# Performance work log

Measured on AMD Instinct MI355X. Metric: run time of the kernel, lower is better.

Reference implementation:

```python
import jax, jax.numpy as jnp
import numpy as np

N, E, D, B = 40000, 100000, 64, 256

def setup_inputs() -> dict:
    key = jax.random.key(0)
    ks = jax.random.split(key, 32)
    p = lambda k, shp: jax.random.normal(k, shp, dtype=jnp.float32) * 0.1
    inp = {
        'n_feat': jax.random.normal(ks[0], (N, 23), dtype=jnp.float32),
        'e_feat': jax.random.normal(ks[1], (E, 19), dtype=jnp.float32),
        'src': jax.random.randint(ks[2], (E,), 0, N, dtype=jnp.int32),
        'dst': jax.random.randint(ks[3], (E,), 0, N, dtype=jnp.int32),
        'node_graph': jnp.sort(jax.random.randint(ks[4], (N,), 0, B, dtype=jnp.int32)),
        'batch_size': B,
        'lin0_w': p(ks[5], (D, 23)), 'lin0_b': p(ks[6], (D,)),
        'en_w1': p(ks[7], (128, 19)), 'en_b1': p(ks[8], (128,)),
        'en_w2': p(ks[9], (D * D, 128)), 'en_b2': p(ks[10], (D * D,)),
        'conv_b': p(ks[11], (D,)),
        'gru_wih': p(ks[12], (3 * D, D)), 'gru_whh': p(ks[13], (3 * D, D)),
        'gru_bih': p(ks[14], (3 * D,)), 'gru_bhh': p(ks[15], (3 * D,)),
        'ls_wih0': p(ks[16], (4 * D, 2 * D)), 'ls_wih12': p(ks[17], (2, 4 * D, D)),
        'ls_whh': p(ks[18], (3, 4 * D, D)),
        'ls_bih': p(ks[19], (3, 4 * D)), 'ls_bhh': p(ks[20], (3, 4 * D)),
        'lin3_w': p(ks[21], (2 * D, 2 * D)), 'lin3_b': p(ks[22], (2 * D,)),
        'pred_w': p(ks[23], (1, 2 * D)), 'pred_b': p(ks[24], (1,)),
    }
    return inp


def _gru_step(x, h, wih, whh, bih, bhh):
    gi = x @ wih.T + bih   # (N, 3D)
    gh = h @ whh.T + bhh
    i_r, i_z, i_n = jnp.split(gi, 3, axis=-1)
    h_r, h_z, h_n = jnp.split(gh, 3, axis=-1)
    r = jax.nn.sigmoid(i_r + h_r)
    z = jax.nn.sigmoid(i_z + h_z)
    n = jnp.tanh(i_n + r * h_n)
    return (1.0 - z) * n + z * h


def _lstm_cell(x, h, c, wih, whh, bih, bhh):
    g = x @ wih.T + bih + h @ whh.T + bhh  # (B, 4D)
    i, f, gg, o = jnp.split(g, 4, axis=-1)
    c2 = jax.nn.sigmoid(f) * c + jax.nn.sigmoid(i) * jnp.tanh(gg)
    h2 = jax.nn.sigmoid(o) * jnp.tanh(c2)
    return h2, c2


def reference(n_feat, e_feat, src, dst, node_graph, batch_size,
              lin0_w, lin0_b, en_w1, en_b1, en_w2, en_b2, conv_b,
              gru_wih, gru_whh, gru_bih, gru_bhh,
              ls_wih0, ls_wih12, ls_whh, ls_bih, ls_bhh,
              lin3_w, lin3_b, pred_w, pred_b):
    d = lin0_b.shape[0]
    n_nodes = n_feat.shape[0]
    # input projection
    out = n_feat @ lin0_w.T + lin0_b                       # (N, D)
    h = out                                                # GRU hidden (1 layer)
    # edge network (same every step) -> per-edge weight matrices
    ew = jax.nn.relu(e_feat @ en_w1.T + en_b1) @ en_w2.T + en_b2
    ew = ew.reshape(-1, d, d)                              # (E, D, D)
    for _ in range(6):
        msg = jnp.einsum('ed,edf->ef', out[src], ew)       # gather + per-edge GEMM
        m = jax.ops.segment_sum(msg, dst, num_segments=n_nodes) + conv_b
        h = _gru_step(m, h, gru_wih, gru_whh, gru_bih, gru_bhh)
        out = h
    # Set2Set pooling
    hs = [jnp.zeros((batch_size, d), jnp.float32) for _ in range(3)]
    cs = [jnp.zeros((batch_size, d), jnp.float32) for _ in range(3)]
    q_star = jnp.zeros((batch_size, 2 * d), jnp.float32)
    for _ in range(6):
        x = q_star
        for l in range(3):
            wih = ls_wih0 if l == 0 else ls_wih12[l - 1]
            hs[l], cs[l] = _lstm_cell(x, hs[l], cs[l], wih, ls_whh[l], ls_bih[l], ls_bhh[l])
            x = hs[l]
        q = x                                              # (B, D)
        e = jnp.sum(out * q[node_graph], axis=-1)          # (N,)
        emax = jax.ops.segment_max(e, node_graph, num_segments=batch_size)
        ee = jnp.exp(e - emax[node_graph])
        esum = jax.ops.segment_sum(ee, node_graph, num_segments=batch_size)
        alpha = (ee / esum[node_graph])[:, None]
        readout = jax.ops.segment_sum(out * alpha, node_graph, num_segments=batch_size)
        q_star = jnp.concatenate([q, readout], axis=-1)
    y = jax.nn.relu(q_star @ lin3_w.T + lin3_b)
    predict = y @ pred_w.T + pred_b
    return h[None], predict
```

## Files before the change

kernel.cpp:

```cpp
#include <hip/hip_runtime.h>

typedef unsigned short u16;
typedef unsigned int u32;
typedef _Float16 f16;
typedef __attribute__((ext_vector_type(8))) _Float16 f16x8;
typedef __attribute__((ext_vector_type(4))) _Float16 f16x4;
typedef __attribute__((ext_vector_type(4))) float f32x4;

#define NN 40000
#define EE 100000
#define DD 64
#define BB 256
#define XTS 136
#define EPB 128

__device__ inline float sigmoidf_(float x){
    return 1.f / (1.f + __expf(-x));
}
__device__ inline float tanhf_(float x){
    x = fmaxf(fminf(x, 15.f), -15.f);
    float e = __expf(2.f * x);
    return (e - 1.f) / (e + 1.f);
}

typedef __attribute__((address_space(3))) unsigned int lds_u32;
typedef __attribute__((address_space(1))) const unsigned int g_u32;
__device__ inline void gload_lds16(const void* g, void* l){
    __builtin_amdgcn_global_load_lds((g_u32*)g, (lds_u32*)l, 16, 0, 0);
}

__global__ __launch_bounds__(256) void prep_kernel(
    const float* __restrict__ en_w2, f16* __restrict__ w2h,
    const float* __restrict__ gru_wih, const float* __restrict__ gru_whh,
    f16* __restrict__ wf16h, f16* __restrict__ wf16l,
    const float* __restrict__ ls_wih0, const float* __restrict__ ls_wih12,
    const float* __restrict__ ls_whh, float* __restrict__ lsT,
    const float* __restrict__ lin3_w, float* __restrict__ lin3T,
    const float* __restrict__ gru_bih, const float* __restrict__ conv_b,
    float* __restrict__ effb,
    const int* __restrict__ node_graph, int* __restrict__ offs)
{
    int i = blockIdx.x * 256 + threadIdx.x;
    if (i < 524288){
        w2h[i] = (f16)en_w2[i];
        return;
    }
    i -= 524288;
    if (i < 49152){
        int sel = i / 12288;
        int r = i % 12288;
        int gg = sel >> 1, islo = sel & 1;
        float v = (gg ? gru_whh : gru_wih)[r];
        f16 hi = (f16)v;
        if (islo) wf16l[gg * 12288 + r] = (f16)(v - (float)hi);
        else      wf16h[gg * 12288 + r] = hi;
        return;
    }
    i -= 49152;
    if (i < 114688){
        float v;
        if (i < 32768){
            int d = i >> 8, g = i & 255;
            v = ls_wih0[g * 128 + d];
        } else if (i < 65536){
            int j = i - 32768;
            int l = j >> 14, r = j & 16383;
            int d = r >> 8, g = r & 255;
            v = ls_wih12[l * 16384 + g * 64 + d];
        } else {
            int j = i - 65536;
            int l = j >> 14, r = j & 16383;
            int d = r >> 8, g = r & 255;
            v = ls_whh[l * 16384 + g * 64 + d];
        }
        lsT[i] = v;
        return;
    }
    i -= 114688;
    if (i < 16384){
        int ii = i >> 7, jj = i & 127;
        lin3T[i] = lin3_w[jj * 128 + ii];
        return;
    }
    i -= 16384;
    if (i < 192){
        float b = gru_bih[i];
        #pragma unroll
        for (int d = 0; d < 64; d++) b += gru_wih[i * 64 + d] * conv_b[d];
        effb[i] = b;
        return;
    }
    i -= 192;
    if (i <= 256){
        int lo = 0, hi = NN;
        while (lo < hi){
            int mid = (lo + hi) >> 1;
            if (node_graph[mid] < i) lo = mid + 1; else hi = mid;
        }
        offs[i] = lo;
        return;
    }
}

__global__ __launch_bounds__(256) void lin0_kernel(
    const float* __restrict__ nf, const float* __restrict__ w,
    const float* __restrict__ b, float* __restrict__ out)
{
    int tid = blockIdx.x * 256 + threadIdx.x;
    int n = tid >> 6, d = tid & 63;
    if (n >= NN) return;
    float acc = b[d];
    const float* nr = nf + (size_t)n * 23;
    const float* wr = w + d * 23;
    #pragma unroll
    for (int j = 0; j < 23; j++) acc = fmaf(nr[j], wr[j], acc);
    out[(size_t)n * 64 + d] = acc;
}

__global__ __launch_bounds__(256) void edge_hidden_kernel(
    const float* __restrict__ ef, const float* __restrict__ w1,
    const float* __restrict__ b1, f16* __restrict__ hidh)
{
    int tid = blockIdx.x * 256 + threadIdx.x;
    int e = tid >> 7, k = tid & 127;
    if (e >= EE) return;
    float acc = b1[k];
    const float* er = ef + (size_t)e * 19;
    const float* wr = w1 + k * 19;
    #pragma unroll
    for (int j = 0; j < 19; j++) acc = fmaf(er[j], wr[j], acc);
    acc = fmaxf(acc, 0.f);
    hidh[(size_t)e * 128 + k] = (f16)acc;
}

__global__ __launch_bounds__(512) void msg_fused_kernel(
    const float* __restrict__ h, const f16* __restrict__ hidh,
    const f16* __restrict__ w2h, const float* __restrict__ b2,
    const int* __restrict__ src, const int* __restrict__ dst,
    float* __restrict__ m)
{
    __shared__ f16 s_xT[64 * XTS];
    __shared__ f16 s_b2f[4096];
    __shared__ int s_dst[EPB];
    __shared__ f16x8 s_t0[1024], s_t1[1024], s_t2[1024];

    const int t = threadIdx.x;
    const int base = blockIdx.x * EPB;
    const int lane = t & 63;
    const int wid = t >> 6;

    int goff[2], lbase[2];
    #pragma unroll
    for (int cc = 0; cc < 2; cc++){
        int s = cc * 512 + wid * 64 + lane;
        int kh = s >> 9;
        int c2 = s & 511;
        int col = c2 >> 3;
        int jj = (c2 & 7) ^ (col & 7);
        goff[cc] = col * 128 + kh * 64 + jj * 8;
        lbase[cc] = cc * 512 + wid * 64;
    }

#define STG_ISSUE(DN, BUF)                                                   \
    {                                                                        \
        const f16* gsrc = w2h + (size_t)(DN) * 8192;                         \
        gload_lds16(gsrc + goff[0], (BUF) + lbase[0]);                       \
        gload_lds16(gsrc + goff[1], (BUF) + lbase[1]);                       \
    }

    f16x8* pb0 = s_t0;
    f16x8* pb1 = s_t1;
    f16x8* pb2 = s_t2;
    STG_ISSUE(0, pb0);
    STG_ISSUE(1, pb1);

    for (int i = t; i < EPB * 64; i += 512){
        int el = i >> 6, f = i & 63;
        int e = base + el;
        float v = 0.f;
        if (e < EE) v = h[(size_t)src[e] * 64 + f];
        s_xT[f * XTS + el] = (f16)v;
    }
    for (int i = t; i < 4096; i += 512) s_b2f[i] = (f16)b2[i];
    if (t < EPB){
        int e = base + t;
        s_dst[t] = (e < EE) ? dst[e] : -1;
    }

    const int eg = wid >> 1;
    const int fp = wid & 1;
    const int r16 = lane & 15;
    const int kg = lane >> 4;
    const int we = eg * 32;
    const int sw = r16 & 7;

    f16x8 ah[2][4];
    #pragma unroll
    for (int mt = 0; mt < 2; mt++){
        int e = base + we + mt * 16 + r16;
        #pragma unroll
        for (int ks = 0; ks < 4; ks++){
            if (e < EE){
                ah[mt][ks] = *(const f16x8*)(hidh + (size_t)e * 128 + ks * 32 + kg * 8);
            } else {
                f16x8 z = {0,0,0,0,0,0,0,0};
                ah[mt][ks] = z;
            }
        }
    }

    f32x4 msg[2][2];
    #pragma unroll
    for (int a = 0; a < 2; a++)
        #pragma unroll
        for (int b = 0; b < 2; b++){
            f32x4 z = {0.f, 0.f, 0.f, 0.f};
            msg[a][b] = z;
        }

    int rslot[2][4];
    #pragma unroll
    for (int ftl = 0; ftl < 2; ftl++){
        int col = fp * 32 + ftl * 16 + r16;
        #pragma unroll
        for (int ks = 0; ks < 4; ks++){
            int j2 = (ks & 1) * 4 + kg;
            rslot[ftl][ks] = (ks >> 1) * 512 + col * 8 + (j2 ^ sw);
        }
    }

    __syncthreads();

    for (int d = 0; d < 64; d++){
        if (d + 2 < 64) STG_ISSUE(d + 2, pb2);
        f32x4 xv[2];
        #pragma unroll
        for (int mt = 0; mt < 2; mt++){
            f16x4 xh = *(const f16x4*)&s_xT[d * XTS + we + mt * 16 + kg * 4];
            #pragma unroll
            for (int r = 0; r < 4; r++) xv[mt][r] = (float)xh[r];
        }
        __builtin_amdgcn_s_setprio(1);
        #pragma unroll
        for (int ftl = 0; ftl < 2; ftl++){
            f16x8 bf0 = pb0[rslot[ftl][0]];
            f16x8 bf1 = pb0[rslot[ftl][1]];
            f16x8 bf2 = pb0[rslot[ftl][2]];
            f16x8 bf3 = pb0[rslot[ftl][3]];
            float b2v = (float)s_b2f[d * 64 + fp * 32 + ftl * 16 + r16];
            #pragma unroll
            for (int mt = 0; mt < 2; mt++){
                f32x4 acc = {b2v, b2v, b2v, b2v};
                acc = __builtin_amdgcn_mfma_f32_16x16x32_f16(ah[mt][0], bf0, acc, 0, 0, 0);
                acc = __builtin_amdgcn_mfma_f32_16x16x32_f16(ah[mt][1], bf1, acc, 0, 0, 0);
                acc = __builtin_amdgcn_mfma_f32_16x16x32_f16(ah[mt][2], bf2, acc, 0, 0, 0);
                acc = __builtin_amdgcn_mfma_f32_16x16x32_f16(ah[mt][3], bf3, acc, 0, 0, 0);
                msg[mt][ftl] = xv[mt] * acc + msg[mt][ftl];
            }
        }
        __builtin_amdgcn_s_setprio(0);
        if (d < 63){
            if (d <= 61) asm volatile("s_waitcnt vmcnt(2)" ::: "memory");
            else         asm volatile("s_waitcnt vmcnt(0)" ::: "memory");
            __builtin_amdgcn_s_barrier();
        }
        f16x8* tmp = pb0; pb0 = pb1; pb1 = pb2; pb2 = tmp;
    }
#undef STG_ISSUE

    #pragma unroll
    for (int mt = 0; mt < 2; mt++){
        #pragma unroll
        for (int r = 0; r < 4; r++){
            int el = we + mt * 16 + kg * 4 + r;
            int dt = s_dst[el];
            if (dt >= 0){
                #pragma unroll
                for (int ftl = 0; ftl < 2; ftl++)
                    atomicAdd(&m[(size_t)dt * 64 + fp * 32 + ftl * 16 + r16],
                              msg[mt][ftl][r]);
            }
        }
    }
}

__global__ __launch_bounds__(256) void gru_mfma_kernel(
    float* __restrict__ m, float* __restrict__ h,
    const f16* __restrict__ wf16h, const f16* __restrict__ wf16l,
    const float* __restrict__ effb, const float* __restrict__ bhh)
{
    __shared__ float s_g[2][32][194];
    const int t = threadIdx.x;
    const int base = blockIdx.x * 32;
    const int lane = t & 63;
    const int wid = t >> 6;
    const int rt = wid & 1;
    const int gg = wid >> 1;
    const int r16 = lane & 15;
    const int kg = lane >> 4;

    const float* __restrict__ X = gg ? h : m;
    int n = base + rt * 16 + r16;

    f16x8 ah[2], al[2];
    #pragma unroll
    for (int ks = 0; ks < 2; ks++){
        const float* xp = X + (size_t)n * 64 + ks * 32 + kg * 8;
        f32x4 v0 = *(const f32x4*)(xp);
        f32x4 v1 = *(const f32x4*)(xp + 4);
        #pragma unroll
        for (int j = 0; j < 4; j++){
            f16 hi0 = (f16)v0[j], hi1 = (f16)v1[j];
            ah[ks][j] = hi0;     ah[ks][4 + j] = hi1;
            al[ks][j] = (f16)(v0[j] - (float)hi0);
            al[ks][4 + j] = (f16)(v1[j] - (float)hi1);
        }
    }

    const f16* __restrict__ wh = wf16h + gg * 12288;
    const f16* __restrict__ wl = wf16l + gg * 12288;
    #pragma unroll
    for (int ct = 0; ct < 12; ct++){
        int g = ct * 16 + r16;
        f16x8 bh0 = *(const f16x8*)(wh + g * 64 + kg * 8);
        f16x8 bh1 = *(const f16x8*)(wh + g * 64 + 32 + kg * 8);
        f16x8 bl0 = *(const f16x8*)(wl + g * 64 + kg * 8);
        f16x8 bl1 = *(const f16x8*)(wl + g * 64 + 32 + kg * 8);
        f32x4 acc = {0.f, 0.f, 0.f, 0.f};
        acc = __builtin_amdgcn_mfma_f32_16x16x32_f16(ah[0], bh0, acc, 0, 0, 0);
        acc = __builtin_amdgcn_mfma_f32_16x16x32_f16(ah[1], bh1, acc, 0, 0, 0);
        acc = __builtin_amdgcn_mfma_f32_16x16x32_f16(ah[0], bl0, acc, 0, 0, 0);
        acc = __builtin_amdgcn_mfma_f32_16x16x32_f16(ah[1], bl1, acc, 0, 0, 0);
        acc = __builtin_amdgcn_mfma_f32_16x16x32_f16(al[0], bh0, acc, 0, 0, 0);
        acc = __builtin_amdgcn_mfma_f32_16x16x32_f16(al[1], bh1, acc, 0, 0, 0);
        #pragma unroll
        for (int r = 0; r < 4; r++)
            s_g[gg][rt * 16 + kg * 4 + r][ct * 16 + r16] = acc[r];
    }
    __syncthreads();

    int node = t >> 3;
    int f0 = (t & 7) * 8;
    int n2 = base + node;
    #pragma unroll
    for (int j = 0; j < 8; j++){
        int f = f0 + j;
        float gir = s_g[0][node][f]       + effb[f];
        float giz = s_g[0][node][64 + f]  + effb[64 + f];
        float gin = s_g[0][node][128 + f] + effb[128 + f];
        float ghr = s_g[1][node][f]       + bhh[f];
        float ghz = s_g[1][node][64 + f]  + bhh[64 + f];
        float ghn = s_g[1][node][128 + f] + bhh[128 + f];
        float r = sigmoidf_(gir + ghr);
        float z = sigmoidf_(giz + ghz);
        float nv = tanhf_(gin + r * ghn);
        size_t hb = (size_t)n2 * 64 + f;
        float hv = h[hb];
        h[hb] = (1.f - z) * nv + z * hv;
        m[hb] = 0.f;
    }
}

__global__ __launch_bounds__(256) void set2set_kernel(
    const float* __restrict__ out, const int* __restrict__ offs,
    const float* __restrict__ lsT, const float* __restrict__ ls_bih,
    const float* __restrict__ ls_bhh, const float* __restrict__ lin3T,
    const float* __restrict__ lin3_b, const float* __restrict__ pred_w,
    const float* __restrict__ pred_b, float* __restrict__ pred_out)
{
    int g = blockIdx.x;
    int t = threadIdx.x;
    __shared__ float s_qstar[128], s_h[3][64], s_c[3][64], s_g[256], s_y[128];
    __shared__ float s_gm[16], s_gw[16];
    __shared__ float s_gr[16][68];
    if (t < 128) s_qstar[t] = 0.f;
    if (t < 192){ s_h[t / 64][t % 64] = 0.f; s_c[t / 64][t % 64] = 0.f; }
    int ns = offs[g], ne = offs[g + 1];
    const int lg = t >> 4;
    const int li = t & 15;
    __syncthreads();

#define LSTM_GATE(L)                                                         \
    __syncthreads();                                                         \
    s_g[t] = acc;                                                            \
    __syncthreads();                                                         \
    if (t < 64){                                                             \
        float iv = s_g[t], fv = s_g[64 + t], gv = s_g[128 + t], ov = s_g[192 + t]; \
        float c2 = sigmoidf_(fv) * s_c[L][t] + sigmoidf_(iv) * tanhf_(gv);   \
        float h2 = sigmoidf_(ov) * tanhf_(c2);                               \
        s_c[L][t] = c2; s_h[L][t] = h2;                                      \
    }                                                                        \
    __syncthreads();

    for (int it = 0; it < 6; it++){
        {
            float acc = ls_bih[t] + ls_bhh[t];
            const float* wx = lsT;
            #pragma unroll 32
            for (int j = 0; j < 128; j++) acc = fmaf(s_qstar[j], wx[j * 256 + t], acc);
            const float* wh = lsT + 65536;
            #pragma unroll 32
            for (int j = 0; j < 64; j++) acc = fmaf(s_h[0][j], wh[j * 256 + t], acc);
            LSTM_GATE(0)
        }
        {
            float acc = ls_bih[256 + t] + ls_bhh[256 + t];
            const float* wx = lsT + 32768;
            #pragma unroll 32
            for (int j = 0; j < 64; j++) acc = fmaf(s_h[0][j], wx[j * 256 + t], acc);
            const float* wh = lsT + 65536 + 16384;
            #pragma unroll 32
            for (int j = 0; j < 64; j++) acc = fmaf(s_h[1][j], wh[j * 256 + t], acc);
            LSTM_GATE(1)
        }
        {
            float acc = ls_bih[512 + t] + ls_bhh[512 + t];
            const float* wx = lsT + 32768 + 16384;
            #pragma unroll 32
            for (int j = 0; j < 64; j++) acc = fmaf(s_h[1][j], wx[j * 256 + t], acc);
            const float* wh = lsT + 65536 + 2 * 16384;
            #pragma unroll 32
            for (int j = 0; j < 64; j++) acc = fmaf(s_h[2][j], wh[j * 256 + t], acc);
            LSTM_GATE(2)
        }
        f32x4 qv = *(const f32x4*)&s_h[2][li * 4];
        f32x4 racc = {0.f, 0.f, 0.f, 0.f};
        float mrun = -3.4e38f, wsum = 0.f;
        for (int n = ns + lg; n < ne; n += 16){
            f32x4 ov = *(const f32x4*)&out[(size_t)n * 64 + li * 4];
            float p = ov[0] * qv[0] + ov[1] * qv[1] + ov[2] * qv[2] + ov[3] * qv[3];
            p += __shfl_xor(p, 1);
            p += __shfl_xor(p, 2);
            p += __shfl_xor(p, 4);
            p += __shfl_xor(p, 8);
            float mn = fmaxf(mrun, p);
            float sc = __expf(mrun - mn);
            float w = __expf(p - mn);
            wsum = fmaf(wsum, sc, w);
            racc = racc * sc + ov * w;
            mrun = mn;
        }
        if (li == 0){ s_gm[lg] = mrun; s_gw[lg] = wsum; }
        *(f32x4*)&s_gr[lg][li * 4] = racc;
        __syncthreads();
        if (t < 64){
            float gmax = -3.4e38f;
            #pragma unroll
            for (int g2 = 0; g2 < 16; g2++) gmax = fmaxf(gmax, s_gm[g2]);
            float gsum = 0.f, ro = 0.f;
            #pragma unroll
            for (int g2 = 0; g2 < 16; g2++){
                float e = __expf(s_gm[g2] - gmax);
                gsum = fmaf(s_gw[g2], e, gsum);
                ro = fmaf(s_gr[g2][t], e, ro);
            }
            ro = (gsum > 0.f) ? ro / gsum : 0.f;
            s_qstar[t] = s_h[2][t];
            s_qstar[64 + t] = ro;
        }
        __syncthreads();
    }
#undef LSTM_GATE
    if (t < 128){
        float acc = lin3_b[t];
        #pragma unroll 32
        for (int i = 0; i < 128; i++) acc = fmaf(s_qstar[i], lin3T[i * 128 + t], acc);
        s_y[t] = fmaxf(acc, 0.f);
    }
    __syncthreads();
    if (t < 64){
        float p = s_y[t] * pred_w[t] + s_y[64 + t] * pred_w[64 + t];
        #pragma unroll
        for (int o = 1; o < 64; o <<= 1) p += __shfl_xor(p, o);
        if (t == 0) pred_out[g] = p + pred_b[0];
    }
}

extern "C" void kernel_launch(void* const* d_in, const int* in_sizes, int n_in,
                              void* d_out, int out_size, void* d_ws, size_t ws_size,
                              hipStream_t stream)
{
    (void)in_sizes; (void)n_in; (void)out_size; (void)ws_size;
    const float* n_feat  = (const float*)d_in[0];
    const float* e_feat  = (const float*)d_in[1];
    const int*   src     = (const int*)d_in[2];
    const int*   dst     = (const int*)d_in[3];
    const int*   node_graph = (const int*)d_in[4];
    const float* lin0_w  = (const float*)d_in[6];
    const float* lin0_b  = (const float*)d_in[7];
    const float* en_w1   = (const float*)d_in[8];
    const float* en_b1   = (const float*)d_in[9];
    const float* en_w2   = (const float*)d_in[10];
    const float* en_b2   = (const float*)d_in[11];
    const float* conv_b  = (const float*)d_in[12];
    const float* gru_wih = (const float*)d_in[13];
    const float* gru_whh = (const float*)d_in[14];
    const float* gru_bih = (const float*)d_in[15];
    const float* gru_bhh = (const float*)d_in[16];
    const float* ls_wih0 = (const float*)d_in[17];
    const float* ls_wih12= (const float*)d_in[18];
    const float* ls_whh  = (const float*)d_in[19];
    const float* ls_bih  = (const float*)d_in[20];
    const float* ls_bhh  = (const float*)d_in[21];
    const float* lin3_w  = (const float*)d_in[22];
    const float* lin3_b  = (const float*)d_in[23];
    const float* pred_w  = (const float*)d_in[24];
    const float* pred_b  = (const float*)d_in[25];

    float* h = (float*)d_out;
    float* pred_out = (float*)d_out + (size_t)NN * 64;

    char* ws = (char*)d_ws;
    f16*   hidh  = (f16*)(ws + 0);
    float* m     = (float*)(ws + 25600000);
    f16*   w2h   = (f16*)(ws + 35840000);
    f16*   wf16h = (f16*)(ws + 36888576);
    f16*   wf16l = (f16*)(ws + 36937728);
    float* lsT   = (float*)(ws + 36986880);
    float* lin3T = (float*)(ws + 37445632);
    float* effb  = (float*)(ws + 37511168);
    int*   offs  = (int*)(ws + 37511936);

    prep_kernel<<<2754, 256, 0, stream>>>(en_w2, w2h, gru_wih, gru_whh,
                                          wf16h, wf16l,
                                          ls_wih0, ls_wih12, ls_whh, lsT,
                                          lin3_w, lin3T, gru_bih, conv_b, effb,
                                          node_graph, offs);
    lin0_kernel<<<(NN * 64) / 256, 256, 0, stream>>>(n_feat, lin0_w, lin0_b, h);
    edge_hidden_kernel<<<(EE * 128) / 256, 256, 0, stream>>>(e_feat, en_w1, en_b1, hidh);
    hipMemsetAsync(m, 0, (size_t)NN * 64 * sizeof(float), stream);

    for (int step = 0; step < 6; step++){
        msg_fused_kernel<<<(EE + EPB - 1) / EPB, 512, 0, stream>>>(h, hidh, w2h,
                                                                   en_b2, src, dst, m);
        gru_mfma_kernel<<<NN / 32, 256, 0, stream>>>(m, h, wf16h, wf16l, effb, gru_bhh);
    }

    set2set_kernel<<<BB, 256, 0, stream>>>(h, offs, lsT, ls_bih, ls_bhh,
                                           lin3T, lin3_b, pred_w, pred_b,
                                           pred_out);
}
```

Before: 1.180 ms.

## Double edges per block in fused message kernel and switch to double-buffered weight staging

Each block now handles 256 edges instead of 128, so every staged 64x128 weight slice for a given output row d is reused across twice as many edges, halving total global weight traffic. The three-buffer async pipeline with explicit vmcnt waits is replaced by a two-buffer scheme that issues the next slice and ends each iteration with a full __syncthreads. The cost is more registers for A fragments and accumulators (lower occupancy), half as many blocks, and possibly less load/compute overlap, since __syncthreads waits on all outstanding loads.

```diff
diff --git a/kernel.cpp b/kernel.cpp
--- a/kernel.cpp
+++ b/kernel.cpp
@@ -11,8 +11,8 @@
 #define EE 100000
 #define DD 64
 #define BB 256
-#define XTS 136
-#define EPB 128
+#define XTS 260
+#define EPB 256
 
 __device__ inline float sigmoidf_(float x){
     return 1.f / (1.f + __expf(-x));
@@ -142,7 +142,7 @@
     __shared__ f16 s_xT[64 * XTS];
     __shared__ f16 s_b2f[4096];
     __shared__ int s_dst[EPB];
-    __shared__ f16x8 s_t0[1024], s_t1[1024], s_t2[1024];
+    __shared__ f16x8 s_bb[2][1024];
 
     const int t = threadIdx.x;
     const int base = blockIdx.x * EPB;
@@ -164,15 +164,11 @@
 #define STG_ISSUE(DN, BUF)                                                   \
     {                                                                        \
         const f16* gsrc = w2h + (size_t)(DN) * 8192;                         \
-        gload_lds16(gsrc + goff[0], (BUF) + lbase[0]);                       \
-        gload_lds16(gsrc + goff[1], (BUF) + lbase[1]);                       \
-    }
-
-    f16x8* pb0 = s_t0;
-    f16x8* pb1 = s_t1;
-    f16x8* pb2 = s_t2;
-    STG_ISSUE(0, pb0);
-    STG_ISSUE(1, pb1);
+        gload_lds16(gsrc + goff[0], &s_bb[BUF][lbase[0]]);                   \
+        gload_lds16(gsrc + goff[1], &s_bb[BUF][lbase[1]]);                   \
+    }
+
+    STG_ISSUE(0, 0);
 
     for (int i = t; i < EPB * 64; i += 512){
         int el = i >> 6, f = i & 63;
@@ -191,12 +187,12 @@
     const int fp = wid & 1;
     const int r16 = lane & 15;
     const int kg = lane >> 4;
-    const int we = eg * 32;
+    const int we = eg * 64;
     const int sw = r16 & 7;
 
-    f16x8 ah[2][4];
-    #pragma unroll
-    for (int mt = 0; mt < 2; mt++){
+    f16x8 ah[4][4];
+    #pragma unroll
+    for (int mt = 0; mt < 4; mt++){
         int e = base + we + mt * 16 + r16;
         #pragma unroll
         for (int ks = 0; ks < 4; ks++){
@@ -209,9 +205,9 @@
         }
     }
 
-    f32x4 msg[2][2];
-    #pragma unroll
-    for (int a = 0; a < 2; a++)
+    f32x4 msg[4][2];
+    #pragma unroll
+    for (int a = 0; a < 4; a++)
         #pragma unroll
         for (int b = 0; b < 2; b++){
             f32x4 z = {0.f, 0.f, 0.f, 0.f};
@@ -232,10 +228,11 @@
     __syncthreads();
 
     for (int d = 0; d < 64; d++){
-        if (d + 2 < 64) STG_ISSUE(d + 2, pb2);
-        f32x4 xv[2];
-        #pragma unroll
-        for (int mt = 0; mt < 2; mt++){
+        int cur = d & 1;
+        if (d < 63) STG_ISSUE(d + 1, cur ^ 1);
+        f32x4 xv[4];
+        #pragma unroll
+        for (int mt = 0; mt < 4; mt++){
             f16x4 xh = *(const f16x4*)&s_xT[d * XTS + we + mt * 16 + kg * 4];
             #pragma unroll
             for (int r = 0; r < 4; r++) xv[mt][r] = (float)xh[r];
@@ -243,13 +240,13 @@
         __builtin_amdgcn_s_setprio(1);
         #pragma unroll
         for (int ftl = 0; ftl < 2; ftl++){
-            f16x8 bf0 = pb0[rslot[ftl][0]];
-            f16x8 bf1 = pb0[rslot[ftl][1]];
-            f16x8 bf2 = pb0[rslot[ftl][2]];
-            f16x8 bf3 = pb0[rslot[ftl][3]];
+            f16x8 bf0 = s_bb[cur][rslot[ftl][0]];
+            f16x8 bf1 = s_bb[cur][rslot[ftl][1]];
+            f16x8 bf2 = s_bb[cur][rslot[ftl][2]];
+            f16x8 bf3 = s_bb[cur][rslot[ftl][3]];
             float b2v = (float)s_b2f[d * 64 + fp * 32 + ftl * 16 + r16];
             #pragma unroll
-            for (int mt = 0; mt < 2; mt++){
+            for (int mt = 0; mt < 4; mt++){
                 f32x4 acc = {b2v, b2v, b2v, b2v};
                 acc = __builtin_amdgcn_mfma_f32_16x16x32_f16(ah[mt][0], bf0, acc, 0, 0, 0);
                 acc = __builtin_amdgcn_mfma_f32_16x16x32_f16(ah[mt][1], bf1, acc, 0, 0, 0);
@@ -259,17 +256,12 @@
             }
         }
         __builtin_amdgcn_s_setprio(0);
-        if (d < 63){
-            if (d <= 61) asm volatile("s_waitcnt vmcnt(2)" ::: "memory");
-            else         asm volatile("s_waitcnt vmcnt(0)" ::: "memory");
-            __builtin_amdgcn_s_barrier();
-        }
-        f16x8* tmp = pb0; pb0 = pb1; pb1 = pb2; pb2 = tmp;
+        __syncthreads();
     }
 #undef STG_ISSUE
 
     #pragma unroll
-    for (int mt = 0; mt < 2; mt++){
+    for (int mt = 0; mt < 4; mt++){
         #pragma unroll
         for (int r = 0; r < 4; r++){
             int el = we + mt * 16 + kg * 4 + r;
```

Result: slower. 1.453 ms (+23.1%).
